# Kernel optimization log

Measured on AMD Instinct MI355X. Metric: run time of the kernel, lower is better.

Reference implementation:

```python
import jax, jax.numpy as jnp
import numpy as np


def to_tb(r, size, base=4):
    # (B, size, size, size) -> (B, (size//base)^3, base, base, base)
    n = size // base
    r = r.reshape(-1, size, size, n, base)
    r = r.transpose(0, 1, 3, 2, 4)
    r = r.reshape(-1, size, n * n, base, base)
    r = r.transpose(0, 2, 1, 3, 4)
    return r.reshape(-1, n ** 3, base, base, base)


def from_tb(r, size, base=4):
    # inverse-ish of to_tb, ends with an extra (0,1,3,2) transpose as in source
    n = size // base
    r = r.reshape(-1, n * n, size, base, base)
    r = r.transpose(0, 2, 1, 3, 4)
    r = r.reshape(-1, size, size, n, base)
    r = r.transpose(0, 1, 3, 2, 4)
    r = r.reshape(-1, size, size, size)
    return r.transpose(0, 1, 3, 2)


def downscale(r, size):
    r = to_tb(r, size)  # base=4
    r = r.sum(axis=(2, 3, 4)) / 64.0
    r = r.reshape(-1, size // 4, size // 4, size // 4)
    return r.transpose(0, 3, 2, 1)


def setup_inputs() -> dict:
    key = jax.random.key(0)
    # (batch=2, level=4, 4, 4, 4^(3*4-2)) with 4*4*1048576 = 256^3 per slice
    x = jax.random.normal(key, (2, 4, 4, 4, 1048576), dtype=jnp.float32)
    return {"x": x}


def reference(x):
    level = x.shape[1]
    xt = jnp.transpose(x, (1, 0, 2, 3, 4))  # (level, batch, 4, 4, ...)
    batch = xt.shape[1]
    d2 = xt.shape[2]
    size_full = 4 ** level
    n3 = (4 ** (level - 1)) ** 3
    ret = []
    for i in range(level):
        r = xt[i]
        r = from_tb(r, size_full, 4 ** i)  # -> (batch, size, size, size)
        for k in range(i):
            r = downscale(r, 4 ** (level - k))
        for _ in range(i):
            r = jnp.tile(r, (1, 4, 4, 4))
        r = to_tb(r, size_full)  # (batch, n3, 4, 4, 4)
        ret.append(r.reshape(-1, n3, 64))
    out = jnp.stack(ret)  # (level, batch, n3, 64)
    out = out.transpose(1, 0, 2, 3).reshape(batch, -1, d2 ** 3)
    return out
```

## Files before the change

### kernel.cpp

```cpp
#include <hip/hip_runtime.h>


__global__ __launch_bounds__(256) void k_stage1(const float* __restrict__ in,
                                                float* __restrict__ out,
                                                float* __restrict__ d1,
                                                float* __restrict__ p2,
                                                float* __restrict__ p3) {
    const int b = blockIdx.y;
    const int bx = blockIdx.x;
    const int tid = threadIdx.x;
    __shared__ float smem[16 * 260];
    const float4* in4 = (const float4*)in;

    if (bx < 4096) {
        const int Y_hi = bx >> 6, Z_hi = bx & 63;
        float4* out4 = (float4*)out;
        const long in_b4 = (long)b * 16777216;
#pragma unroll
        for (int k = 0; k < 4; ++k) {
            int idx = k * 256 + tid;
            int r = idx >> 6;
            int col4 = idx & 63;
            int Y = Y_hi * 4 + (r >> 2), Z = Z_hi * 4 + (r & 3);
            float4 v = in4[in_b4 + (long)Y * 16384 + Z * 64 + col4];
            *(float4*)&smem[r * 260 + col4 * 4] = v;
        }
        __syncthreads();
        const long out_b4 = (long)b * 16777216 + (long)Z_hi * 65536 + Y_hi * 1024;
#pragma unroll
        for (int k = 0; k < 4; ++k) {
            int idx = k * 256 + tid;
            int X = ((idx >> 4) << 2) + ((tid >> 2) & 3);
            int row0 = (tid & 3) * 4;
            float4 v;
            v.x = smem[(row0 + 0) * 260 + X];
            v.y = smem[(row0 + 1) * 260 + X];
            v.z = smem[(row0 + 2) * 260 + X];
            v.w = smem[(row0 + 3) * 260 + X];
            out4[out_b4 + idx] = v;
        }
    } else if (bx < 6144) {
        const int blk = bx - 4096;
        const int tlow = blk >> 1;
        const int kh = blk & 1;
        const long base4 = (long)b * 16777216 + 4194304;
        float acc[2] = {0.f, 0.f};
        for (int dz = 0; dz < 4; ++dz) {
            long rb = base4 + (long)(dz * 1024 + tlow) * 1024;
#pragma unroll
            for (int kk = 0; kk < 2; ++kk) {
                int k = kh * 2 + kk;
                float4 v = in4[rb + k * 256 + tid];
                acc[kk] += v.x + v.y + v.z + v.w;
            }
        }
#pragma unroll
        for (int kk = 0; kk < 2; ++kk) {
            acc[kk] += __shfl_xor(acc[kk], 4);
            acc[kk] += __shfl_xor(acc[kk], 8);
        }
        if ((tid & 12) == 0) {
            int yp = tlow >> 4;
            int zp = ((tlow & 15) << 2) + (tid & 3);
#pragma unroll
            for (int kk = 0; kk < 2; ++kk) {
                int xp = (kh * 2 + kk) * 16 + (tid >> 4);
                d1[b * 262144 + xp * 4096 + yp * 64 + zp] = acc[kk] * (1.0f / 64.0f);
            }
        }
    } else if (bx < 8192) {
        const int blk = bx - 6144;
        const int g = blk & 7, cell = blk >> 3;
        const int yp = cell >> 4, xp = cell & 15;
        const long base4 = (long)b * 16777216 + 2 * 4194304 + yp * 16384 + xp * 1024;
        float acc = 0.f;
        for (int dzi = 0; dzi < 2; ++dzi) {
            long rb = base4 + (long)(g * 2 + dzi) * 262144;
#pragma unroll
            for (int k = 0; k < 4; ++k) {
                float4 v = in4[rb + k * 256 + tid];
                acc += v.x + v.y + v.z + v.w;
            }
        }
        acc += __shfl_xor(acc, 1);
        acc += __shfl_xor(acc, 2);
        float* red = smem;
        if ((tid & 3) == 0) red[tid >> 2] = acc;
        __syncthreads();
        if (tid < 16) {
            float s = red[tid] + red[16 + tid] + red[32 + tid] + red[48 + tid];
            p2[(b * 8 + g) * 4096 + xp * 256 + yp * 16 + tid] = s;
        }
    } else {
        const int blk = bx - 8192;
        const int kc = blk & 7;
        const int orig = blk >> 3;
        const int xp = orig >> 6, hi = (orig >> 2) & 15, dxg = orig & 3;
        const long base4 = (long)b * 16777216 + 3 * 4194304 +
                           (long)hi * 262144 + xp * 65536 + dxg * 16384;
        float acc = 0.f;
        for (int kk = 0; kk < 8; ++kk) {
            float4 v = in4[base4 + (kc * 8 + kk) * 256 + tid];
            acc += v.x + v.y + v.z + v.w;
        }
        acc += __shfl_xor(acc, 1);
        acc += __shfl_xor(acc, 2);
        acc += __shfl_xor(acc, 4);
        acc += __shfl_xor(acc, 8);
        float* red = smem;
        if ((tid & 15) == 0) red[tid >> 4] = acc;
        __syncthreads();
        if (tid < 16) {
            int G = (hi * 4 + dxg) * 8 + kc;
            p3[((b * 4 + xp) * 512 + G) * 16 + tid] = red[tid];
        }
    }
}

__global__ __launch_bounds__(256) void k_combine(const float* __restrict__ p2,
                                                 const float* __restrict__ p3,
                                                 float* __restrict__ d2,
                                                 float* __restrict__ d3) {
    const int bid = blockIdx.x;
    const int tid = threadIdx.x;
    if (bid < 32) {
        int idx = bid * 256 + tid;
        int b = idx >> 12, r = idx & 4095;
        float s = 0.f;
#pragma unroll
        for (int g = 0; g < 8; ++g) s += p2[(b * 8 + g) * 4096 + r];
        d2[idx] = s * (1.0f / 4096.0f);
    } else {
        int v = bid - 32;
        int b = v >> 2, xp = v & 3;
        int c = tid & 15, gp = tid >> 4;
        const float* pb = p3 + (long)((b * 4 + xp) * 512) * 16 + c;
        float s = 0.f;
#pragma unroll
        for (int j = 0; j < 32; ++j) s += pb[(gp * 32 + j) * 16];
        __shared__ float red[256];
        red[gp * 16 + c] = s;
        __syncthreads();
        if (tid < 16) {
            float t = 0.f;
#pragma unroll
            for (int g = 0; g < 16; ++g) t += red[g * 16 + tid];
            d3[b * 64 + xp * 16 + tid] = t * (1.0f / 262144.0f);
        }
    }
}

__global__ __launch_bounds__(256) void k_stage2(const float* __restrict__ d1,
                                                const float* __restrict__ d2,
                                                const float* __restrict__ d3,
                                                float* __restrict__ out) {
    const int b = blockIdx.y;
    const int bx = blockIdx.x;
    const int tid = threadIdx.x;
    __shared__ float4 smem4[1024];
    float4* out4 = (float4*)out;

    if (bx < 4096) {
        const float4* d14 = (const float4*)d1;
        const long ob = (long)b * 16777216 + 4194304;
        const int d1b = b * 65536;
#pragma unroll
        for (int k = 0; k < 4; ++k) {
            int o4 = bx * 1024 + k * 256 + tid;
            int u = o4 >> 4;
            int Xl = (o4 >> 2) & 3, Yl = o4 & 3;
            int Xh = u & 63, Yh = (u >> 6) & 63, Zh = u >> 12;
            int x = (Xh & 15) * 4 + Xl, y = (Yh & 15) * 4 + Yl;
            out4[ob + o4] = d14[d1b + x * 1024 + y * 16 + (Zh & 15)];
        }
    } else if (bx < 8192) {
        const int blk = bx - 4096;
        const float4* d24 = (const float4*)d2;
#pragma unroll
        for (int j = 0; j < 4; ++j) smem4[j * 256 + tid] = d24[b * 1024 + j * 256 + tid];
        __syncthreads();
        const long ob = (long)b * 16777216 + 2 * 4194304;
#pragma unroll
        for (int k = 0; k < 4; ++k) {
            int o4 = blk * 1024 + k * 256 + tid;
            int u = o4 >> 4;
            int Xl = (o4 >> 2) & 3, Yl = o4 & 3;
            int Xh = u & 63, Yh = (u >> 6) & 63, Zh = u >> 12;
            int x = (Xh & 3) * 4 + Xl, y = (Yh & 3) * 4 + Yl;
            out4[ob + o4] = smem4[x * 64 + y * 4 + (Zh & 3)];
        }
    } else {
        const int blk = bx - 8192;
        const float4* d34 = (const float4*)d3;
        const float4 v = d34[b * 16 + (tid & 15)];
        const long ob = (long)b * 16777216 + 3 * 4194304;
#pragma unroll
        for (int k = 0; k < 4; ++k)
            out4[ob + blk * 1024 + k * 256 + tid] = v;
    }
}

extern "C" void kernel_launch(void* const* d_in, const int* in_sizes, int n_in,
                              void* d_out, int out_size, void* d_ws, size_t ws_size,
                              hipStream_t stream) {
    const float* in = (const float*)d_in[0];
    float* out = (float*)d_out;
    float* ws = (float*)d_ws;
    float* d1 = ws;
    float* p2 = ws + 524288;
    float* p3 = ws + 524288 + 65536;
    float* d2 = ws + 524288 + 65536 + 65536;
    float* d3 = ws + 524288 + 65536 + 65536 + 8192;
    k_stage1 <<<dim3(10240, 2), 256, 0, stream>>>(in, out, d1, p2, p3);
    k_combine<<<40, 256, 0, stream>>>(p2, p3, d2, d3);
    k_stage2 <<<dim3(12288, 2), 256, 0, stream>>>(d1, d2, d3, out);
}
```

Baseline: 224.7 us.

## Split permute from reductions and use nontemporal loads/stores throughout

Moves the level-0 permutation out of the reduction kernel into its own kernel, launched after the combine step. All streaming global loads and output stores now use nontemporal builtins so they bypass cache retention. The broadcast of d2 now reads global memory directly instead of staging it in shared memory. The split adds one kernel launch, and the permute no longer overlaps with the reductions inside a single grid.

```diff
diff --git a/kernel.cpp b/kernel.cpp
--- a/kernel.cpp
+++ b/kernel.cpp
@@ -1,56 +1,28 @@
 #include <hip/hip_runtime.h>
 
 
-__global__ __launch_bounds__(256) void k_stage1(const float* __restrict__ in,
-                                                float* __restrict__ out,
+typedef float f4 __attribute__((ext_vector_type(4)));
+
+__global__ __launch_bounds__(256) void k_reduce(const float* __restrict__ in,
                                                 float* __restrict__ d1,
                                                 float* __restrict__ p2,
                                                 float* __restrict__ p3) {
     const int b = blockIdx.y;
     const int bx = blockIdx.x;
     const int tid = threadIdx.x;
-    __shared__ float smem[16 * 260];
-    const float4* in4 = (const float4*)in;
-
-    if (bx < 4096) {
-        const int Y_hi = bx >> 6, Z_hi = bx & 63;
-        float4* out4 = (float4*)out;
-        const long in_b4 = (long)b * 16777216;
-#pragma unroll
-        for (int k = 0; k < 4; ++k) {
-            int idx = k * 256 + tid;
-            int r = idx >> 6;
-            int col4 = idx & 63;
-            int Y = Y_hi * 4 + (r >> 2), Z = Z_hi * 4 + (r & 3);
-            float4 v = in4[in_b4 + (long)Y * 16384 + Z * 64 + col4];
-            *(float4*)&smem[r * 260 + col4 * 4] = v;
-        }
-        __syncthreads();
-        const long out_b4 = (long)b * 16777216 + (long)Z_hi * 65536 + Y_hi * 1024;
-#pragma unroll
-        for (int k = 0; k < 4; ++k) {
-            int idx = k * 256 + tid;
-            int X = ((idx >> 4) << 2) + ((tid >> 2) & 3);
-            int row0 = (tid & 3) * 4;
-            float4 v;
-            v.x = smem[(row0 + 0) * 260 + X];
-            v.y = smem[(row0 + 1) * 260 + X];
-            v.z = smem[(row0 + 2) * 260 + X];
-            v.w = smem[(row0 + 3) * 260 + X];
-            out4[out_b4 + idx] = v;
-        }
-    } else if (bx < 6144) {
-        const int blk = bx - 4096;
-        const int tlow = blk >> 1;
-        const int kh = blk & 1;
+    __shared__ float red[64];
+    const f4* in4 = (const f4*)in;
+
+    if (bx < 2048) {
+        const int tlow = bx >> 1;
+        const int kh = bx & 1;
         const long base4 = (long)b * 16777216 + 4194304;
         float acc[2] = {0.f, 0.f};
         for (int dz = 0; dz < 4; ++dz) {
             long rb = base4 + (long)(dz * 1024 + tlow) * 1024;
 #pragma unroll
             for (int kk = 0; kk < 2; ++kk) {
-                int k = kh * 2 + kk;
-                float4 v = in4[rb + k * 256 + tid];
+                f4 v = __builtin_nontemporal_load(&in4[rb + (kh * 2 + kk) * 256 + tid]);
                 acc[kk] += v.x + v.y + v.z + v.w;
             }
         }
@@ -68,8 +40,8 @@
                 d1[b * 262144 + xp * 4096 + yp * 64 + zp] = acc[kk] * (1.0f / 64.0f);
             }
         }
-    } else if (bx < 8192) {
-        const int blk = bx - 6144;
+    } else if (bx < 4096) {
+        const int blk = bx - 2048;
         const int g = blk & 7, cell = blk >> 3;
         const int yp = cell >> 4, xp = cell & 15;
         const long base4 = (long)b * 16777216 + 2 * 4194304 + yp * 16384 + xp * 1024;
@@ -78,13 +50,12 @@
             long rb = base4 + (long)(g * 2 + dzi) * 262144;
 #pragma unroll
             for (int k = 0; k < 4; ++k) {
-                float4 v = in4[rb + k * 256 + tid];
+                f4 v = __builtin_nontemporal_load(&in4[rb + k * 256 + tid]);
                 acc += v.x + v.y + v.z + v.w;
             }
         }
         acc += __shfl_xor(acc, 1);
         acc += __shfl_xor(acc, 2);
-        float* red = smem;
         if ((tid & 3) == 0) red[tid >> 2] = acc;
         __syncthreads();
         if (tid < 16) {
@@ -92,7 +63,7 @@
             p2[(b * 8 + g) * 4096 + xp * 256 + yp * 16 + tid] = s;
         }
     } else {
-        const int blk = bx - 8192;
+        const int blk = bx - 4096;
         const int kc = blk & 7;
         const int orig = blk >> 3;
         const int xp = orig >> 6, hi = (orig >> 2) & 15, dxg = orig & 3;
@@ -100,14 +71,13 @@
                            (long)hi * 262144 + xp * 65536 + dxg * 16384;
         float acc = 0.f;
         for (int kk = 0; kk < 8; ++kk) {
-            float4 v = in4[base4 + (kc * 8 + kk) * 256 + tid];
+            f4 v = __builtin_nontemporal_load(&in4[base4 + (kc * 8 + kk) * 256 + tid]);
             acc += v.x + v.y + v.z + v.w;
         }
         acc += __shfl_xor(acc, 1);
         acc += __shfl_xor(acc, 2);
         acc += __shfl_xor(acc, 4);
         acc += __shfl_xor(acc, 8);
-        float* red = smem;
         if ((tid & 15) == 0) red[tid >> 4] = acc;
         __syncthreads();
         if (tid < 16) {
@@ -150,18 +120,51 @@
     }
 }
 
-__global__ __launch_bounds__(256) void k_stage2(const float* __restrict__ d1,
-                                                const float* __restrict__ d2,
-                                                const float* __restrict__ d3,
-                                                float* __restrict__ out) {
+__global__ __launch_bounds__(256) void k_perm(const float* __restrict__ in,
+                                              float* __restrict__ out) {
+    const int b = blockIdx.y;
+    const int Y_hi = blockIdx.x >> 6, Z_hi = blockIdx.x & 63;
+    const int tid = threadIdx.x;
+    __shared__ float lds[16 * 260];
+    const f4* in4 = (const f4*)in;
+    f4* out4 = (f4*)out;
+    const long in_b4 = (long)b * 16777216;
+#pragma unroll
+    for (int k = 0; k < 4; ++k) {
+        int idx = k * 256 + tid;
+        int r = idx >> 6;
+        int col4 = idx & 63;
+        int Y = Y_hi * 4 + (r >> 2), Z = Z_hi * 4 + (r & 3);
+        f4 v = __builtin_nontemporal_load(&in4[in_b4 + (long)Y * 16384 + Z * 64 + col4]);
+        *(f4*)&lds[r * 260 + col4 * 4] = v;
+    }
+    __syncthreads();
+    const long out_b4 = (long)b * 16777216 + (long)Z_hi * 65536 + Y_hi * 1024;
+#pragma unroll
+    for (int k = 0; k < 4; ++k) {
+        int idx = k * 256 + tid;
+        int X = ((idx >> 4) << 2) + ((tid >> 2) & 3);
+        int row0 = (tid & 3) * 4;
+        f4 v;
+        v.x = lds[(row0 + 0) * 260 + X];
+        v.y = lds[(row0 + 1) * 260 + X];
+        v.z = lds[(row0 + 2) * 260 + X];
+        v.w = lds[(row0 + 3) * 260 + X];
+        __builtin_nontemporal_store(v, &out4[out_b4 + idx]);
+    }
+}
+
+__global__ __launch_bounds__(256) void k_bcast(const float* __restrict__ d1,
+                                               const float* __restrict__ d2,
+                                               const float* __restrict__ d3,
+                                               float* __restrict__ out) {
     const int b = blockIdx.y;
     const int bx = blockIdx.x;
     const int tid = threadIdx.x;
-    __shared__ float4 smem4[1024];
-    float4* out4 = (float4*)out;
+    f4* out4 = (f4*)out;
 
     if (bx < 4096) {
-        const float4* d14 = (const float4*)d1;
+        const f4* d14 = (const f4*)d1;
         const long ob = (long)b * 16777216 + 4194304;
         const int d1b = b * 65536;
 #pragma unroll
@@ -171,14 +174,12 @@
             int Xl = (o4 >> 2) & 3, Yl = o4 & 3;
             int Xh = u & 63, Yh = (u >> 6) & 63, Zh = u >> 12;
             int x = (Xh & 15) * 4 + Xl, y = (Yh & 15) * 4 + Yl;
-            out4[ob + o4] = d14[d1b + x * 1024 + y * 16 + (Zh & 15)];
+            f4 v = d14[d1b + x * 1024 + y * 16 + (Zh & 15)];
+            __builtin_nontemporal_store(v, &out4[ob + o4]);
         }
     } else if (bx < 8192) {
         const int blk = bx - 4096;
-        const float4* d24 = (const float4*)d2;
-#pragma unroll
-        for (int j = 0; j < 4; ++j) smem4[j * 256 + tid] = d24[b * 1024 + j * 256 + tid];
-        __syncthreads();
+        const f4* d24 = (const f4*)d2;
         const long ob = (long)b * 16777216 + 2 * 4194304;
 #pragma unroll
         for (int k = 0; k < 4; ++k) {
@@ -187,16 +188,17 @@
             int Xl = (o4 >> 2) & 3, Yl = o4 & 3;
             int Xh = u & 63, Yh = (u >> 6) & 63, Zh = u >> 12;
             int x = (Xh & 3) * 4 + Xl, y = (Yh & 3) * 4 + Yl;
-            out4[ob + o4] = smem4[x * 64 + y * 4 + (Zh & 3)];
+            f4 v = d24[b * 1024 + x * 64 + y * 4 + (Zh & 3)];
+            __builtin_nontemporal_store(v, &out4[ob + o4]);
         }
     } else {
         const int blk = bx - 8192;
-        const float4* d34 = (const float4*)d3;
-        const float4 v = d34[b * 16 + (tid & 15)];
+        const f4* d34 = (const f4*)d3;
+        const f4 v = d34[b * 16 + (tid & 15)];
         const long ob = (long)b * 16777216 + 3 * 4194304;
 #pragma unroll
         for (int k = 0; k < 4; ++k)
-            out4[ob + blk * 1024 + k * 256 + tid] = v;
+            __builtin_nontemporal_store(v, &out4[ob + blk * 1024 + k * 256 + tid]);
     }
 }
 
@@ -211,7 +213,8 @@
     float* p3 = ws + 524288 + 65536;
     float* d2 = ws + 524288 + 65536 + 65536;
     float* d3 = ws + 524288 + 65536 + 65536 + 8192;
-    k_stage1 <<<dim3(10240, 2), 256, 0, stream>>>(in, out, d1, p2, p3);
+    k_reduce <<<dim3(6144, 2),  256, 0, stream>>>(in, d1, p2, p3);
     k_combine<<<40, 256, 0, stream>>>(p2, p3, d2, d3);
-    k_stage2 <<<dim3(12288, 2), 256, 0, stream>>>(d1, d2, d3, out);
-}
+    k_perm   <<<dim3(4096, 2),  256, 0, stream>>>(in, out);
+    k_bcast  <<<dim3(12288, 2), 256, 0, stream>>>(d1, d2, d3, out);
+}
```

Result: faster. 187.1 us (-16.7%).
